# Performance work log

Measured on AMD Instinct MI355X. Metric: run time of the kernel, lower is better.

Reference implementation:

```python
import jax, jax.numpy as jnp
import numpy as np

N_HEAD = 8
LN_EPS = 1e-6


def setup_inputs() -> dict:
    key = jax.random.key(0)
    ks = jax.random.split(key, 6)
    B, S, D = 4, 2048, 256  # D = hidden_size*2 = input_dim
    sc = 1.0 / np.sqrt(D)
    return {
        "inputs": jax.random.normal(ks[0], (B, S, D), jnp.float32),
        "Wq": jax.random.normal(ks[1], (D, D), jnp.float32) * sc,
        "Wk": jax.random.normal(ks[2], (D, D), jnp.float32) * sc,
        "Wv": jax.random.normal(ks[3], (D, D), jnp.float32) * sc,
        "Wf": jax.random.normal(ks[4], (D, D), jnp.float32) * sc,
        "bf": jnp.zeros((D,), jnp.float32),
        "gamma": jnp.ones((D,), jnp.float32),
        "beta": jnp.zeros((D,), jnp.float32),
    }


def reference(inputs, Wq, Wk, Wv, Wf, bf, gamma, beta):
    B, S, D = inputs.shape
    H = N_HEAD
    dh = D // H
    # Projections (torch Linear: x @ W.T), no bias for Q/K/V
    Q = (inputs @ Wq.T).reshape(B, S, H, dh)
    K = (inputs @ Wk.T).reshape(B, S, H, dh)
    V = (inputs @ Wv.T).reshape(B, S, H, dh)
    # NOTE: original scales by sqrt(K.shape[1]) == sqrt(seq_len), not sqrt(dh)
    scale = 1.0 / jnp.sqrt(jnp.float32(S)).astype(inputs.dtype)
    scores = jnp.einsum("bqhd,bkhd->bhqk", Q, K) * scale  # [B,H,S,S]
    attn = jax.nn.softmax(scores, axis=-1)
    out = jnp.einsum("bhqk,bkhd->bqhd", attn, V).reshape(B, S, D)
    out = out @ Wf.T + bf
    # residual + LayerNorm(eps=1e-6)
    x = inputs + out
    mu = jnp.mean(x, axis=-1, keepdims=True)
    var = jnp.mean(jnp.square(x - mu), axis=-1, keepdims=True)
    return (x - mu) * jax.lax.rsqrt(var + LN_EPS) * gamma + beta
```

## Files before the change

kernel.cpp:

```cpp
#include <hip/hip_runtime.h>
#include <hip/hip_bf16.h>

typedef __attribute__((ext_vector_type(8))) short short8;
typedef __attribute__((ext_vector_type(4))) float f32x4;
typedef __attribute__((ext_vector_type(16))) float f32x16;

#define DEVI __device__ __forceinline__

DEVI unsigned short f2bf(float f) {
  union { float f; unsigned int u; } v; v.f = f;
  unsigned int r = v.u + 0x7fffu + ((v.u >> 16) & 1u);
  return (unsigned short)(r >> 16);
}

#define GLDS16(gp, lp)                                                         \
  __builtin_amdgcn_global_load_lds(                                            \
      (const __attribute__((address_space(1))) unsigned int*)(uintptr_t)(gp),  \
      (__attribute__((address_space(3))) unsigned int*)(uintptr_t)(lp), 16, 0, 0)

#define SB 4
#define SS 2048
#define SD 256
#define SH 8
#define SDH 32
#define SM 8192

#define QSCALE 0.0318793654f

#define XBF_OFF 0
#define W_OFF   (SM * SD)
#define Q_OFF   (W_OFF + 4 * SD * SD)
#define K_OFF   (Q_OFF + SM * SD)
#define VT_OFF  (K_OFF + SM * SD)
#define AO_OFF  (VT_OFF + SM * SD)

__global__ __launch_bounds__(256) void convert_k(
    const float* __restrict__ X, const float* __restrict__ Wq,
    const float* __restrict__ Wk, const float* __restrict__ Wv,
    const float* __restrict__ Wf, unsigned short* __restrict__ ws) {
  const int XN = SM * SD;
  const int WN = SD * SD;
  int i4 = (blockIdx.x * 256 + threadIdx.x) * 4;
  const float* src; unsigned short* dst; int idx;
  if (i4 < XN)             { src = X;  dst = ws + XBF_OFF;      idx = i4; }
  else if (i4 < XN + WN)   { src = Wq; dst = ws + W_OFF;        idx = i4 - XN; }
  else if (i4 < XN + 2*WN) { src = Wk; dst = ws + W_OFF + WN;   idx = i4 - XN - WN; }
  else if (i4 < XN + 3*WN) { src = Wv; dst = ws + W_OFF + 2*WN; idx = i4 - XN - 2*WN; }
  else if (i4 < XN + 4*WN) { src = Wf; dst = ws + W_OFF + 3*WN; idx = i4 - XN - 3*WN; }
  else return;
  float4 v = *reinterpret_cast<const float4*>(src + idx);
  unsigned short o[4] = { f2bf(v.x), f2bf(v.y), f2bf(v.z), f2bf(v.w) };
  *reinterpret_cast<uint2*>(dst + idx) = *reinterpret_cast<const uint2*>(o);
}

__global__ __launch_bounds__(256) void qkv_k(const unsigned short* __restrict__ ws_c,
                                             unsigned short* __restrict__ ws) {
  __shared__ __align__(16) unsigned short Atile[128][72];
  __shared__ __align__(16) unsigned short Btile[128][72];
  const unsigned short* Xb = ws_c + XBF_OFF;
  const unsigned short* Wall = ws_c + W_OFF;
  int tid = threadIdx.x, w = tid >> 6, lane = tid & 63, g = lane >> 4, r = lane & 15;
  int m0 = blockIdx.x * 128, n0 = blockIdx.y * 128;
  int wr = (w >> 1) * 64, wc = (w & 1) * 64;
  f32x4 acc[4][4] = {};
  int srow = tid >> 3, scol = (tid & 7) * 8;
  short8 a[4], b[4];
#pragma unroll
  for (int p = 0; p < 4; ++p) {
    a[p] = *reinterpret_cast<const short8*>(Xb + (m0 + srow + p * 32) * SD + scol);
    b[p] = *reinterpret_cast<const short8*>(Wall + (n0 + srow + p * 32) * SD + scol);
  }
  for (int k0 = 0; k0 < SD; k0 += 64) {
    __syncthreads();
#pragma unroll
    for (int p = 0; p < 4; ++p) {
      *reinterpret_cast<short8*>(&Atile[srow + p * 32][scol]) = a[p];
      *reinterpret_cast<short8*>(&Btile[srow + p * 32][scol]) = b[p];
    }
    __syncthreads();
    if (k0 + 64 < SD) {
#pragma unroll
      for (int p = 0; p < 4; ++p) {
        a[p] = *reinterpret_cast<const short8*>(Xb + (m0 + srow + p * 32) * SD + k0 + 64 + scol);
        b[p] = *reinterpret_cast<const short8*>(Wall + (n0 + srow + p * 32) * SD + k0 + 64 + scol);
      }
    }
#pragma unroll
    for (int ks = 0; ks < 2; ++ks) {
      short8 af[4], bf[4];
#pragma unroll
      for (int i = 0; i < 4; ++i)
        af[i] = *reinterpret_cast<const short8*>(&Atile[wr + i * 16 + r][ks * 32 + g * 8]);
#pragma unroll
      for (int j = 0; j < 4; ++j)
        bf[j] = *reinterpret_cast<const short8*>(&Btile[wc + j * 16 + r][ks * 32 + g * 8]);
#pragma unroll
      for (int i = 0; i < 4; ++i)
#pragma unroll
        for (int j = 0; j < 4; ++j)
          acc[i][j] = __builtin_amdgcn_mfma_f32_16x16x32_bf16(af[i], bf[j], acc[i][j], 0, 0, 0);
    }
  }
  int z = n0 >> 8;
  int nbase = n0 & 255;
  if (z < 2) {
    unsigned short* out = ws + (z == 0 ? Q_OFF : K_OFF);
    float qs = (z == 0) ? QSCALE : 1.0f;
#pragma unroll
    for (int j = 0; j < 4; ++j) {
      int col = nbase + wc + j * 16 + r;
      int h = col >> 5, d = col & 31;
#pragma unroll
      for (int i = 0; i < 4; ++i) {
#pragma unroll
        for (int jj = 0; jj < 4; ++jj) {
          int m = m0 + wr + i * 16 + g * 4 + jj;
          int b_ = m >> 11, s = m & 2047;
          out[(((b_ << 3) + h) * SS + s) * SDH + d] = f2bf(acc[i][j][jj] * qs);
        }
      }
    }
  } else {
    unsigned short* out = ws + VT_OFF;
#pragma unroll
    for (int j = 0; j < 4; ++j) {
      int col = nbase + wc + j * 16 + r;
      int h = col >> 5, d = col & 31;
#pragma unroll
      for (int i = 0; i < 4; ++i) {
        int m = m0 + wr + i * 16 + g * 4;
        int b_ = m >> 11, s = m & 2047;
        unsigned short o4[4];
#pragma unroll
        for (int jj = 0; jj < 4; ++jj) o4[jj] = f2bf(acc[i][j][jj]);
        *reinterpret_cast<uint2*>(out + ((((b_ << 3) + h) << 5) + d) * SS + s) =
            *reinterpret_cast<const uint2*>(o4);
      }
    }
  }
}

__global__ __launch_bounds__(512, 4) void attn_k(const unsigned short* __restrict__ ws_c,
                                                 unsigned short* __restrict__ ws) {
  __shared__ __align__(16) unsigned short Kb[2][2][64 * 32];
  __shared__ __align__(16) unsigned short Vb[2][2][32 * 64];
  int tid = threadIdx.x, w = tid >> 6, lane = tid & 63;
  int wg = w >> 2, wl = w & 3, gtid = tid & 255;
  int n32 = lane & 31, hi = lane >> 5;
  int wgid = ((blockIdx.x & 7) << 6) + (blockIdx.x >> 3);
  int bh = wgid >> 4, qb = wgid & 15;
  int q0 = qb * 128 + wl * 32;
  const unsigned short* Qh = ws_c + Q_OFF + bh * (SS * SDH);
  const unsigned short* Kg = ws_c + K_OFF + (bh * SS + wg * 1024) * SDH;
  const unsigned short* Vg = ws_c + VT_OFF + bh * (SDH * SS) + wg * 1024;
  short8 qB0 = *reinterpret_cast<const short8*>(Qh + (q0 + n32) * SDH + 8 * hi);
  short8 qB1 = *reinterpret_cast<const short8*>(Qh + (q0 + n32) * SDH + 16 + 8 * hi);
  int krow = gtid >> 2, kch = (gtid & 3) ^ (krow & 3);
  const unsigned short* gK = Kg + krow * SDH + kch * 8;
  int vrow = gtid >> 3, vch = (gtid & 7) ^ (vrow & 7);
  const unsigned short* gV = Vg + vrow * SS + vch * 8;
  int wv = gtid >> 6;
  unsigned short* lK[2] = { &Kb[wg][0][wv * 512], &Kb[wg][1][wv * 512] };
  unsigned short* lV[2] = { &Vb[wg][0][wv * 512], &Vb[wg][1][wv * 512] };
  GLDS16(gK, lK[0]);
  GLDS16(gV, lV[0]);
  f32x16 O = {};
  float Lacc = 0.f;
  for (int t = 0; t < 16; ++t) {
    const unsigned short* Kbase = &Kb[wg][t & 1][0];
    const unsigned short* Vbase = &Vb[wg][t & 1][0];
    if (t < 15) {
      GLDS16(gK + (t + 1) * 64 * SDH, lK[(t + 1) & 1]);
      GLDS16(gV + (t + 1) * 64, lV[(t + 1) & 1]);
      asm volatile("s_waitcnt vmcnt(2)" ::: "memory");
    } else {
      asm volatile("s_waitcnt vmcnt(0)" ::: "memory");
    }
    __builtin_amdgcn_s_barrier();
#pragma unroll
    for (int s = 0; s < 2; ++s) {
      int R0 = s * 32 + n32;
      short8 kA0 = *reinterpret_cast<const short8*>(Kbase + R0 * 32 + ((hi ^ (n32 & 3)) * 8));
      short8 kA1 = *reinterpret_cast<const short8*>(Kbase + R0 * 32 + (((2 + hi) ^ (n32 & 3)) * 8));
      short8 vB0 = *reinterpret_cast<const short8*>(Vbase + n32 * 64 + (((s * 4 + hi) ^ (n32 & 7)) * 8));
      short8 vB1 = *reinterpret_cast<const short8*>(Vbase + n32 * 64 + (((s * 4 + 2 + hi) ^ (n32 & 7)) * 8));
      f32x16 acc = {};
      __builtin_amdgcn_s_setprio(1);
      acc = __builtin_amdgcn_mfma_f32_32x32x16_bf16(kA0, qB0, acc, 0, 0, 0);
      acc = __builtin_amdgcn_mfma_f32_32x32x16_bf16(kA1, qB1, acc, 0, 0, 0);
      __builtin_amdgcn_s_setprio(0);
#pragma unroll
      for (int i = 0; i < 16; ++i) acc[i] = __builtin_amdgcn_exp2f(acc[i]);
      float s0 = 0.f, s1 = 0.f;
#pragma unroll
      for (int i = 0; i < 8; ++i) { s0 += acc[2 * i]; s1 += acc[2 * i + 1]; }
      Lacc += s0 + s1;
      unsigned int pk[8];
#pragma unroll
      for (int i = 0; i < 8; ++i) {
        unsigned int rr;
        asm("v_cvt_pk_bf16_f32 %0, %1, %2" : "=v"(rr) : "v"(acc[2 * i]), "v"(acc[2 * i + 1]));
        pk[i] = rr;
      }
      asm("v_permlane32_swap_b32 %0, %1" : "+v"(pk[0]), "+v"(pk[2]));
      asm("v_permlane32_swap_b32 %0, %1" : "+v"(pk[1]), "+v"(pk[3]));
      asm("v_permlane32_swap_b32 %0, %1" : "+v"(pk[4]), "+v"(pk[6]));
      asm("v_permlane32_swap_b32 %0, %1" : "+v"(pk[5]), "+v"(pk[7]));
      union { unsigned int u[4]; short8 sv; } A1, A2;
      A1.u[0] = pk[0]; A1.u[1] = pk[1]; A1.u[2] = pk[2]; A1.u[3] = pk[3];
      A2.u[0] = pk[4]; A2.u[1] = pk[5]; A2.u[2] = pk[6]; A2.u[3] = pk[7];
      __builtin_amdgcn_s_setprio(1);
      O = __builtin_amdgcn_mfma_f32_32x32x16_bf16(A1.sv, vB0, O, 0, 0, 0);
      O = __builtin_amdgcn_mfma_f32_32x32x16_bf16(A2.sv, vB1, O, 0, 0, 0);
      __builtin_amdgcn_s_setprio(0);
    }
    __builtin_amdgcn_s_barrier();
  }
  __syncthreads();
  float* OCp = reinterpret_cast<float*>(&Kb[0][0][0]);
  float* LCp = reinterpret_cast<float*>(&Vb[0][0][0]);
  if (wg == 1) {
#pragma unroll
    for (int i = 0; i < 16; ++i) OCp[(wl * 64 + lane) * 16 + i] = O[i];
    LCp[wl * 64 + lane] = Lacc;
  }
  __syncthreads();
  if (wg == 0) {
#pragma unroll
    for (int i = 0; i < 16; ++i) O[i] += OCp[(wl * 64 + lane) * 16 + i];
    Lacc += LCp[wl * 64 + lane];
    float Lt = Lacc + __shfl_xor(Lacc, 32);
    float* Linv = LCp + 256 + wl * 32;
    if (lane < 32) Linv[n32] = 1.0f / Lt;
    int b = bh >> 3, h = bh & 7;
    unsigned short* AO = ws + AO_OFF;
#pragma unroll
    for (int rr = 0; rr < 16; ++rr) {
      int q = (rr & 3) + 8 * (rr >> 2) + 4 * hi;
      AO[(b * SS + q0 + q) * SD + h * SDH + n32] = f2bf(O[rr] * Linv[q]);
    }
  }
}

__global__ __launch_bounds__(256) void final_k(
    const unsigned short* __restrict__ ws_c, const float* __restrict__ X,
    const float* __restrict__ bfv, const float* __restrict__ gamma,
    const float* __restrict__ beta, float* __restrict__ out) {
  __shared__ __align__(16) unsigned short Al[32][72];
  __shared__ __align__(16) unsigned short Bl[256][72];
  __shared__ float Cl[32][257];
  const unsigned short* AO = ws_c + AO_OFF;
  const unsigned short* Wf = ws_c + W_OFF + 3 * (SD * SD);
  int tid = threadIdx.x, w = tid >> 6, lane = tid & 63, g = lane >> 4, r = lane & 15;
  int m0 = blockIdx.x * 32;
  f32x4 acc[2][4] = {};
  int arow = tid >> 3, acol = (tid & 7) * 8;
  for (int k0 = 0; k0 < SD; k0 += 64) {
    short8 av = *reinterpret_cast<const short8*>(AO + (m0 + arow) * SD + k0 + acol);
    short8 bv[8];
#pragma unroll
    for (int i = 0; i < 8; i++)
      bv[i] = *reinterpret_cast<const short8*>(Wf + (i * 32 + arow) * SD + k0 + acol);
    __syncthreads();
    *reinterpret_cast<short8*>(&Al[arow][acol]) = av;
#pragma unroll
    for (int i = 0; i < 8; i++)
      *reinterpret_cast<short8*>(&Bl[i * 32 + arow][acol]) = bv[i];
    __syncthreads();
#pragma unroll
    for (int ks = 0; ks < 2; ks++) {
      short8 af0 = *reinterpret_cast<const short8*>(&Al[r][ks * 32 + g * 8]);
      short8 af1 = *reinterpret_cast<const short8*>(&Al[16 + r][ks * 32 + g * 8]);
#pragma unroll
      for (int nt = 0; nt < 4; nt++) {
        short8 bb = *reinterpret_cast<const short8*>(&Bl[w * 64 + nt * 16 + r][ks * 32 + g * 8]);
        acc[0][nt] = __builtin_amdgcn_mfma_f32_16x16x32_bf16(af0, bb, acc[0][nt], 0, 0, 0);
        acc[1][nt] = __builtin_amdgcn_mfma_f32_16x16x32_bf16(af1, bb, acc[1][nt], 0, 0, 0);
      }
    }
  }
#pragma unroll
  for (int rt = 0; rt < 2; rt++)
#pragma unroll
    for (int nt = 0; nt < 4; nt++)
#pragma unroll
      for (int j = 0; j < 4; j++)
        Cl[rt * 16 + g * 4 + j][w * 64 + nt * 16 + r] = acc[rt][nt][j];
  __syncthreads();
  int row = tid >> 3, sub = tid & 7;
  int m = m0 + row;
  float x[32];
  float sum = 0.f, sumsq = 0.f;
#pragma unroll
  for (int i = 0; i < 8; i++) {
    int col = sub * 32 + i * 4;
    float4 xv = *reinterpret_cast<const float4*>(X + m * SD + col);
    float4 bb = *reinterpret_cast<const float4*>(bfv + col);
    x[i * 4 + 0] = Cl[row][col + 0] + xv.x + bb.x;
    x[i * 4 + 1] = Cl[row][col + 1] + xv.y + bb.y;
    x[i * 4 + 2] = Cl[row][col + 2] + xv.z + bb.z;
    x[i * 4 + 3] = Cl[row][col + 3] + xv.w + bb.w;
  }
#pragma unroll
  for (int c = 0; c < 32; c++) { sum += x[c]; sumsq += x[c] * x[c]; }
  sum += __shfl_xor(sum, 1);  sumsq += __shfl_xor(sumsq, 1);
  sum += __shfl_xor(sum, 2);  sumsq += __shfl_xor(sumsq, 2);
  sum += __shfl_xor(sum, 4);  sumsq += __shfl_xor(sumsq, 4);
  float mean = sum * (1.0f / 256.0f);
  float var = sumsq * (1.0f / 256.0f) - mean * mean;
  float rstd = rsqrtf(var + 1e-6f);
#pragma unroll
  for (int i = 0; i < 8; i++) {
    int col = sub * 32 + i * 4;
    float4 gv = *reinterpret_cast<const float4*>(gamma + col);
    float4 bv2 = *reinterpret_cast<const float4*>(beta + col);
    float4 ov;
    ov.x = (x[i * 4 + 0] - mean) * rstd * gv.x + bv2.x;
    ov.y = (x[i * 4 + 1] - mean) * rstd * gv.y + bv2.y;
    ov.z = (x[i * 4 + 2] - mean) * rstd * gv.z + bv2.z;
    ov.w = (x[i * 4 + 3] - mean) * rstd * gv.w + bv2.w;
    *reinterpret_cast<float4*>(out + m * SD + col) = ov;
  }
}

extern "C" void kernel_launch(void* const* d_in, const int* in_sizes, int n_in,
                              void* d_out, int out_size, void* d_ws, size_t ws_size,
                              hipStream_t stream) {
  const float* X  = (const float*)d_in[0];
  const float* Wq = (const float*)d_in[1];
  const float* Wk = (const float*)d_in[2];
  const float* Wv = (const float*)d_in[3];
  const float* Wf = (const float*)d_in[4];
  const float* bf = (const float*)d_in[5];
  const float* gm = (const float*)d_in[6];
  const float* bt = (const float*)d_in[7];
  float* out = (float*)d_out;
  unsigned short* ws = (unsigned short*)d_ws;

  convert_k<<<2304, 256, 0, stream>>>(X, Wq, Wk, Wv, Wf, ws);
  qkv_k<<<dim3(64, 6), 256, 0, stream>>>(ws, ws);
  attn_k<<<dim3(512), 512, 0, stream>>>(ws, ws);
  final_k<<<256, 256, 0, stream>>>(ws, X, bf, gm, bt, out);
}
```

Baseline: 59.43 us.

## Stage QKV projection epilogue through LDS and interleave attention subtiles

The QKV projection epilogue now writes accumulators into shared memory in two passes and then emits coalesced 16-byte global stores for Q, K and the transposed V. Before, it did scattered 2-byte and 8-byte stores. Separately, the attention inner loop is manually unrolled so the two 32-key subtiles' QK MFMAs, exp2 and pack steps are interleaved, giving more independent MFMA work per step. The cost is extra barriers and LDS traffic in the epilogue, plus higher register pressure in the attention loop, which runs under launch bounds of 512 threads and 4 blocks.

```diff
diff --git a/kernel.cpp b/kernel.cpp
--- a/kernel.cpp
+++ b/kernel.cpp
@@ -103,38 +103,58 @@
   }
   int z = n0 >> 8;
   int nbase = n0 & 255;
-  if (z < 2) {
-    unsigned short* out = ws + (z == 0 ? Q_OFF : K_OFF);
-    float qs = (z == 0) ? QSCALE : 1.0f;
-#pragma unroll
-    for (int j = 0; j < 4; ++j) {
-      int col = nbase + wc + j * 16 + r;
-      int h = col >> 5, d = col & 31;
-#pragma unroll
-      for (int i = 0; i < 4; ++i) {
-#pragma unroll
-        for (int jj = 0; jj < 4; ++jj) {
-          int m = m0 + wr + i * 16 + g * 4 + jj;
-          int b_ = m >> 11, s = m & 2047;
-          out[(((b_ << 3) + h) * SS + s) * SDH + d] = f2bf(acc[i][j][jj] * qs);
-        }
-      }
-    }
-  } else {
-    unsigned short* out = ws + VT_OFF;
-#pragma unroll
-    for (int j = 0; j < 4; ++j) {
-      int col = nbase + wc + j * 16 + r;
-      int h = col >> 5, d = col & 31;
-#pragma unroll
-      for (int i = 0; i < 4; ++i) {
-        int m = m0 + wr + i * 16 + g * 4;
-        int b_ = m >> 11, s = m & 2047;
-        unsigned short o4[4];
-#pragma unroll
-        for (int jj = 0; jj < 4; ++jj) o4[jj] = f2bf(acc[i][j][jj]);
-        *reinterpret_cast<uint2*>(out + ((((b_ << 3) + h) << 5) + d) * SS + s) =
-            *reinterpret_cast<const uint2*>(o4);
+  int b_ = m0 >> 11, sbase = m0 & 2047;
+  float qs = (z == 0) ? QSCALE : 1.0f;
+  unsigned short* Vt = &Btile[0][0];
+#pragma unroll
+  for (int p = 0; p < 2; ++p) {
+    __syncthreads();
+    if ((w & 1) == p) {
+      if (z < 2) {
+#pragma unroll
+        for (int i = 0; i < 4; ++i)
+#pragma unroll
+          for (int j = 0; j < 4; ++j)
+#pragma unroll
+            for (int jj = 0; jj < 4; ++jj)
+              Atile[wr + i * 16 + g * 4 + jj][j * 16 + r] = f2bf(acc[i][j][jj] * qs);
+      } else {
+#pragma unroll
+        for (int i = 0; i < 4; ++i)
+#pragma unroll
+          for (int j = 0; j < 4; ++j) {
+            unsigned short o4[4];
+#pragma unroll
+            for (int jj = 0; jj < 4; ++jj) o4[jj] = f2bf(acc[i][j][jj]);
+            *reinterpret_cast<uint2*>(&Vt[(j * 16 + r) * 136 + wr + i * 16 + g * 4]) =
+                *reinterpret_cast<const uint2*>(o4);
+          }
+      }
+    }
+    __syncthreads();
+    if (z < 2) {
+      unsigned short* out = ws + (z == 0 ? Q_OFF : K_OFF);
+      int h0 = (nbase + p * 64) >> 5;
+#pragma unroll
+      for (int it = 0; it < 4; ++it) {
+        int c = it * 256 + tid;
+        int m = c >> 3, cr = c & 7, hl = cr >> 2, ch = cr & 3;
+        short8 val = *reinterpret_cast<const short8*>(&Atile[m][hl * 32 + ch * 8]);
+        int h = h0 + hl;
+        *reinterpret_cast<short8*>(
+            out + (((b_ << 3) + h) * SS + sbase + m) * SDH + ch * 8) = val;
+      }
+    } else {
+      unsigned short* out = ws + VT_OFF;
+      int nb = nbase + p * 64;
+#pragma unroll
+      for (int it = 0; it < 4; ++it) {
+        int c = it * 256 + tid;
+        int nl = c >> 4, ch = c & 15;
+        short8 val = *reinterpret_cast<const short8*>(&Vt[nl * 136 + ch * 8]);
+        int col = nb + nl, h = col >> 5, d = col & 31;
+        *reinterpret_cast<short8*>(
+            out + ((((b_ << 3) + h) << 5) + d) * SS + sbase + ch * 8) = val;
       }
     }
   }
@@ -177,43 +197,56 @@
       asm volatile("s_waitcnt vmcnt(0)" ::: "memory");
     }
     __builtin_amdgcn_s_barrier();
-#pragma unroll
-    for (int s = 0; s < 2; ++s) {
-      int R0 = s * 32 + n32;
-      short8 kA0 = *reinterpret_cast<const short8*>(Kbase + R0 * 32 + ((hi ^ (n32 & 3)) * 8));
-      short8 kA1 = *reinterpret_cast<const short8*>(Kbase + R0 * 32 + (((2 + hi) ^ (n32 & 3)) * 8));
-      short8 vB0 = *reinterpret_cast<const short8*>(Vbase + n32 * 64 + (((s * 4 + hi) ^ (n32 & 7)) * 8));
-      short8 vB1 = *reinterpret_cast<const short8*>(Vbase + n32 * 64 + (((s * 4 + 2 + hi) ^ (n32 & 7)) * 8));
-      f32x16 acc = {};
-      __builtin_amdgcn_s_setprio(1);
-      acc = __builtin_amdgcn_mfma_f32_32x32x16_bf16(kA0, qB0, acc, 0, 0, 0);
-      acc = __builtin_amdgcn_mfma_f32_32x32x16_bf16(kA1, qB1, acc, 0, 0, 0);
-      __builtin_amdgcn_s_setprio(0);
-#pragma unroll
-      for (int i = 0; i < 16; ++i) acc[i] = __builtin_amdgcn_exp2f(acc[i]);
-      float s0 = 0.f, s1 = 0.f;
-#pragma unroll
-      for (int i = 0; i < 8; ++i) { s0 += acc[2 * i]; s1 += acc[2 * i + 1]; }
-      Lacc += s0 + s1;
-      unsigned int pk[8];
-#pragma unroll
-      for (int i = 0; i < 8; ++i) {
-        unsigned int rr;
-        asm("v_cvt_pk_bf16_f32 %0, %1, %2" : "=v"(rr) : "v"(acc[2 * i]), "v"(acc[2 * i + 1]));
-        pk[i] = rr;
-      }
-      asm("v_permlane32_swap_b32 %0, %1" : "+v"(pk[0]), "+v"(pk[2]));
-      asm("v_permlane32_swap_b32 %0, %1" : "+v"(pk[1]), "+v"(pk[3]));
-      asm("v_permlane32_swap_b32 %0, %1" : "+v"(pk[4]), "+v"(pk[6]));
-      asm("v_permlane32_swap_b32 %0, %1" : "+v"(pk[5]), "+v"(pk[7]));
-      union { unsigned int u[4]; short8 sv; } A1, A2;
-      A1.u[0] = pk[0]; A1.u[1] = pk[1]; A1.u[2] = pk[2]; A1.u[3] = pk[3];
-      A2.u[0] = pk[4]; A2.u[1] = pk[5]; A2.u[2] = pk[6]; A2.u[3] = pk[7];
-      __builtin_amdgcn_s_setprio(1);
-      O = __builtin_amdgcn_mfma_f32_32x32x16_bf16(A1.sv, vB0, O, 0, 0, 0);
-      O = __builtin_amdgcn_mfma_f32_32x32x16_bf16(A2.sv, vB1, O, 0, 0, 0);
-      __builtin_amdgcn_s_setprio(0);
-    }
+    short8 kA00 = *reinterpret_cast<const short8*>(Kbase + n32 * 32 + ((hi ^ (n32 & 3)) * 8));
+    short8 kA01 = *reinterpret_cast<const short8*>(Kbase + n32 * 32 + (((2 + hi) ^ (n32 & 3)) * 8));
+    short8 kA10 = *reinterpret_cast<const short8*>(Kbase + (32 + n32) * 32 + ((hi ^ (n32 & 3)) * 8));
+    short8 kA11 = *reinterpret_cast<const short8*>(Kbase + (32 + n32) * 32 + (((2 + hi) ^ (n32 & 3)) * 8));
+    f32x16 a0 = {}, a1 = {};
+    __builtin_amdgcn_s_setprio(1);
+    a0 = __builtin_amdgcn_mfma_f32_32x32x16_bf16(kA00, qB0, a0, 0, 0, 0);
+    a1 = __builtin_amdgcn_mfma_f32_32x32x16_bf16(kA10, qB0, a1, 0, 0, 0);
+    a0 = __builtin_amdgcn_mfma_f32_32x32x16_bf16(kA01, qB1, a0, 0, 0, 0);
+    a1 = __builtin_amdgcn_mfma_f32_32x32x16_bf16(kA11, qB1, a1, 0, 0, 0);
+    __builtin_amdgcn_s_setprio(0);
+#pragma unroll
+    for (int i = 0; i < 16; ++i) a0[i] = __builtin_amdgcn_exp2f(a0[i]);
+#pragma unroll
+    for (int i = 0; i < 16; ++i) a1[i] = __builtin_amdgcn_exp2f(a1[i]);
+    float s0 = 0.f, s1 = 0.f;
+#pragma unroll
+    for (int i = 0; i < 8; ++i) { s0 += a0[2 * i] + a1[2 * i]; s1 += a0[2 * i + 1] + a1[2 * i + 1]; }
+    Lacc += s0 + s1;
+    unsigned int pk0[8], pk1[8];
+#pragma unroll
+    for (int i = 0; i < 8; ++i) {
+      unsigned int r0, r1;
+      asm("v_cvt_pk_bf16_f32 %0, %1, %2" : "=v"(r0) : "v"(a0[2 * i]), "v"(a0[2 * i + 1]));
+      asm("v_cvt_pk_bf16_f32 %0, %1, %2" : "=v"(r1) : "v"(a1[2 * i]), "v"(a1[2 * i + 1]));
+      pk0[i] = r0; pk1[i] = r1;
+    }
+    asm("v_permlane32_swap_b32 %0, %1" : "+v"(pk0[0]), "+v"(pk0[2]));
+    asm("v_permlane32_swap_b32 %0, %1" : "+v"(pk0[1]), "+v"(pk0[3]));
+    asm("v_permlane32_swap_b32 %0, %1" : "+v"(pk0[4]), "+v"(pk0[6]));
+    asm("v_permlane32_swap_b32 %0, %1" : "+v"(pk0[5]), "+v"(pk0[7]));
+    asm("v_permlane32_swap_b32 %0, %1" : "+v"(pk1[0]), "+v"(pk1[2]));
+    asm("v_permlane32_swap_b32 %0, %1" : "+v"(pk1[1]), "+v"(pk1[3]));
+    asm("v_permlane32_swap_b32 %0, %1" : "+v"(pk1[4]), "+v"(pk1[6]));
+    asm("v_permlane32_swap_b32 %0, %1" : "+v"(pk1[5]), "+v"(pk1[7]));
+    union { unsigned int u[4]; short8 sv; } A10, A20, A11, A21;
+    A10.u[0] = pk0[0]; A10.u[1] = pk0[1]; A10.u[2] = pk0[2]; A10.u[3] = pk0[3];
+    A20.u[0] = pk0[4]; A20.u[1] = pk0[5]; A20.u[2] = pk0[6]; A20.u[3] = pk0[7];
+    A11.u[0] = pk1[0]; A11.u[1] = pk1[1]; A11.u[2] = pk1[2]; A11.u[3] = pk1[3];
+    A21.u[0] = pk1[4]; A21.u[1] = pk1[5]; A21.u[2] = pk1[6]; A21.u[3] = pk1[7];
+    short8 vB00 = *reinterpret_cast<const short8*>(Vbase + n32 * 64 + ((hi ^ (n32 & 7)) * 8));
+    short8 vB01 = *reinterpret_cast<const short8*>(Vbase + n32 * 64 + (((2 + hi) ^ (n32 & 7)) * 8));
+    short8 vB10 = *reinterpret_cast<const short8*>(Vbase + n32 * 64 + (((4 + hi) ^ (n32 & 7)) * 8));
+    short8 vB11 = *reinterpret_cast<const short8*>(Vbase + n32 * 64 + (((6 + hi) ^ (n32 & 7)) * 8));
+    __builtin_amdgcn_s_setprio(1);
+    O = __builtin_amdgcn_mfma_f32_32x32x16_bf16(A10.sv, vB00, O, 0, 0, 0);
+    O = __builtin_amdgcn_mfma_f32_32x32x16_bf16(A20.sv, vB01, O, 0, 0, 0);
+    O = __builtin_amdgcn_mfma_f32_32x32x16_bf16(A11.sv, vB10, O, 0, 0, 0);
+    O = __builtin_amdgcn_mfma_f32_32x32x16_bf16(A21.sv, vB11, O, 0, 0, 0);
+    __builtin_amdgcn_s_setprio(0);
     __builtin_amdgcn_s_barrier();
   }
   __syncthreads();
```

Result: no change. 59.09 us (-0.6%).
